# Kernel optimization log

Hardware: AMD Instinct MI355X
Metric: run time of the kernel (lower is better)

The kernel has to match this reference:

```python
import jax, jax.numpy as jnp
import numpy as np

DIM_MODEL = 512
KDIM = 64
NUM_FREQS = 70


def setup_inputs() -> dict:
    key = jax.random.key(0)
    ks = jax.random.split(key, 8)
    B, N = 8, 2048
    src = jax.random.normal(ks[0], (B, N, DIM_MODEL), dtype=jnp.float32)
    bias_tensor = jax.random.normal(ks[1], (N, N, 4), dtype=jnp.float32)
    multiplier = jax.random.uniform(ks[2], (B, N, N), dtype=jnp.float32)
    # f_theta_lc params
    W_r = jax.random.normal(ks[3], (NUM_FREQS, 2), dtype=jnp.float32)  # std=1.0 init
    C = jnp.ones((NUM_FREQS,), dtype=jnp.float32)
    log_p = jnp.float32(0.0)
    # Xavier-uniform attention projections (torch Linear weight layout [out, in])
    lim = float(np.sqrt(6.0 / (DIM_MODEL + KDIM)))
    W_q = jax.random.uniform(ks[4], (KDIM, DIM_MODEL), minval=-lim, maxval=lim, dtype=jnp.float32)
    W_k = jax.random.uniform(ks[5], (KDIM, DIM_MODEL), minval=-lim, maxval=lim, dtype=jnp.float32)
    W_v = jax.random.uniform(ks[6], (KDIM, DIM_MODEL), minval=-lim, maxval=lim, dtype=jnp.float32)
    s = jnp.float32(1.0)
    return {"src": src, "bias_tensor": bias_tensor, "multiplier": multiplier,
            "W_r": W_r, "C": C, "log_p": log_p,
            "W_q": W_q, "W_k": W_k, "W_v": W_v, "s": s}


def _f_theta(bias_tensor, W_r, C, log_p):
    # bias_tensor: [N, N, 4]; W_r: [F, 2]
    k1 = jnp.einsum('nmi,fi->nmf', bias_tensor[:, :, 0:2], W_r)
    k2 = jnp.einsum('nmi,fi->nmf', bias_tensor[:, :, 2:4], W_r)
    diff = jnp.cos(k1) + jnp.sin(k1) - jnp.cos(k2) - jnp.sin(k2)
    sigma = jnp.abs(jnp.sum(diff * C, axis=-1))  # [N, N]
    p = jnp.clip(jnp.exp(log_p), 0.5, 3.0)
    return jnp.exp(-jnp.power(sigma + 1e-6, p))


def reference(src, bias_tensor, multiplier, W_r, C, log_p, W_q, W_k, W_v, s):
    B = _f_theta(bias_tensor, W_r, C, log_p)  # [N, N]
    Q = jnp.einsum('bnd,kd->bnk', src, W_q)
    K = jnp.einsum('bnd,kd->bnk', src, W_k)
    V = jnp.einsum('bnd,kd->bnk', src, W_v)
    denom = jnp.sqrt(jnp.float32(KDIM))
    logits = (jnp.einsum('bnk,bmk->bnm', Q, K) + B[None]) / denom
    logits = logits * (s * multiplier)
    attn = jax.nn.softmax(logits, axis=-1)
    return jnp.einsum('bnm,bmk->bnk', attn, V)
```

## Files before the change

### kernel.cpp

```cpp
#include <hip/hip_runtime.h>
#include <hip/hip_bf16.h>

#define N_SEQ 2048
#define NB 8
#define DM 512
#define KD 64
#define NF 70

#define TG 512
#define TRANGE 6.5f
#define TSCL (511.0f / 13.0f)
#define TOFS (6.5f * TSCL)

typedef float f32x4 __attribute__((ext_vector_type(4)));
typedef short v8s  __attribute__((ext_vector_type(8)));

__device__ __forceinline__ ushort f2bf(float x) {
    uint u = __float_as_uint(x);
    return (ushort)((u + 0x7FFFu + ((u >> 16) & 1u)) >> 16);
}
__device__ __forceinline__ float bf2f(ushort h) {
    return __uint_as_float(((uint)h) << 16);
}
__device__ __forceinline__ uint cvtpk(float lo, float hi) {
    uint r;
    asm("v_cvt_pk_bf16_f32 %0, %1, %2" : "=v"(r) : "v"(lo), "v"(hi));
    return r;
}

__global__ __launch_bounds__(256) void tbuild_kernel(
    const float* __restrict__ Wr, const float* __restrict__ Cc,
    float4* __restrict__ T4)
{
    const float SQ2 = 1.41421356237309504880f;
    const float R2PI = 0.15915494309189533577f;
    int idx = blockIdx.x * 256 + threadIdx.x;
    int j = idx >> 9, i = idx & (TG - 1);
    const float h = 2.0f * TRANGE / (TG - 1);
    float y = -TRANGE + j * h;
    float x = -TRANGE + i * h;
    float g = 0.f;
    for (int f = 0; f < NF; ++f) {
        float w0 = Wr[2*f] * R2PI, w1 = Wr[2*f+1] * R2PI, cf = Cc[f];
        float k = __builtin_amdgcn_fractf(fmaf(x, w0, fmaf(y, w1, 0.125f)));
        g = fmaf(cf, __builtin_amdgcn_sinf(k), g);
    }
    g *= SQ2;
    float* T = (float*)T4;
    int ix = idx;
    T[4*ix + 0] = g;
    if (i > 0)               T[4*(ix - 1) + 1] = g;
    if (i == TG - 1)         T[4*ix + 1] = g;
    if (j > 0)               T[4*(ix - TG) + 2] = g;
    if (j == TG - 1)         T[4*ix + 2] = g;
    if (i > 0 && j > 0)      T[4*(ix - TG - 1) + 3] = g;
    if (i == TG - 1 && j > 0)         T[4*(ix - TG) + 3] = g;
    if (j == TG - 1 && i > 0)         T[4*(ix - 1) + 3] = g;
    if (i == TG - 1 && j == TG - 1)   T[4*ix + 3] = g;
}

#define QKV_BLOCKS 512

__global__ __launch_bounds__(256) void fat_kernel(
    const float* __restrict__ src, const float* __restrict__ Wq,
    const float* __restrict__ Wk, const float* __restrict__ Wv,
    ushort* __restrict__ Qh, ushort* __restrict__ Ql,
    ushort* __restrict__ Kh, ushort* __restrict__ VhT,
    const float* __restrict__ bias, const float4* __restrict__ T4,
    const float* __restrict__ logp, ushort* __restrict__ Bm)
{
    __shared__ ushort sS[32][72];
    __shared__ ushort sW[192][72];
    int tid = threadIdx.x;

    if (blockIdx.x < QKV_BLOCKS) {
        int lane = tid & 63, w = tid >> 6;
        int wr = w >> 1, wc = w & 1;
        int g = lane >> 4, ln = lane & 15;
        int row0 = blockIdx.x * 32;

        f32x4 acc[6];
#pragma unroll
        for (int t = 0; t < 6; ++t) acc[t] = {0.f, 0.f, 0.f, 0.f};

        for (int kc = 0; kc < 8; ++kc) {
            int k0 = kc * 64;
            __syncthreads();
            {
                int r = tid >> 3, c8 = (tid & 7) * 8;
                float4 f0 = *(const float4*)&src[(long)(row0 + r)*DM + k0 + c8];
                float4 f1 = *(const float4*)&src[(long)(row0 + r)*DM + k0 + c8 + 4];
                uint4 pk = make_uint4(cvtpk(f0.x, f0.y), cvtpk(f0.z, f0.w),
                                      cvtpk(f1.x, f1.y), cvtpk(f1.z, f1.w));
                *(uint4*)&sS[r][c8] = pk;
            }
            {
#pragma unroll
                for (int j = 0; j < 6; ++j) {
                    int slot = tid + j*256;
                    int r = slot >> 3, c8 = (slot & 7) * 8;
                    const float* Wp = (r < 64) ? Wq : (r < 128 ? Wk : Wv);
                    int rr = r & 63;
                    float4 f0 = *(const float4*)&Wp[(long)rr*DM + k0 + c8];
                    float4 f1 = *(const float4*)&Wp[(long)rr*DM + k0 + c8 + 4];
                    uint4 pk = make_uint4(cvtpk(f0.x, f0.y), cvtpk(f0.z, f0.w),
                                          cvtpk(f1.x, f1.y), cvtpk(f1.z, f1.w));
                    *(uint4*)&sW[r][c8] = pk;
                }
            }
            __syncthreads();
#pragma unroll
            for (int kw = 0; kw < 2; ++kw) {
                v8s bsrc = *(const v8s*)&sS[16*wr + ln][32*kw + 8*g];
#pragma unroll
                for (int t = 0; t < 6; ++t) {
                    v8s aw = *(const v8s*)&sW[96*wc + 16*t + ln][32*kw + 8*g];
                    acc[t] = __builtin_amdgcn_mfma_f32_16x16x32_bf16(aw, bsrc, acc[t], 0, 0, 0);
                }
            }
        }
        int n = row0 + 16*wr + ln;
        int bb = n >> 11, nn = n & 2047;
#pragma unroll
        for (int t = 0; t < 6; ++t) {
            int c0 = 96*wc + 16*t + 4*g;
            f32x4 v = acc[t];
            uint2 hp = make_uint2(cvtpk(v[0], v[1]), cvtpk(v[2], v[3]));
            if (c0 < 64) {
                *(uint2*)&Qh[(long)n*KD + c0] = hp;
                float h0 = __uint_as_float(hp.x << 16);
                float h1 = __uint_as_float(hp.x & 0xFFFF0000u);
                float h2 = __uint_as_float(hp.y << 16);
                float h3 = __uint_as_float(hp.y & 0xFFFF0000u);
                uint2 lp = make_uint2(cvtpk(v[0]-h0, v[1]-h1), cvtpk(v[2]-h2, v[3]-h3));
                *(uint2*)&Ql[(long)n*KD + c0] = lp;
            } else if (c0 < 128) {
                *(uint2*)&Kh[(long)n*KD + (c0 - 64)] = hp;
            } else {
                int kv = c0 - 128;
                VhT[((long)bb*KD + kv + 0)*N_SEQ + nn] = (ushort)(hp.x & 0xFFFFu);
                VhT[((long)bb*KD + kv + 1)*N_SEQ + nn] = (ushort)(hp.x >> 16);
                VhT[((long)bb*KD + kv + 2)*N_SEQ + nn] = (ushort)(hp.y & 0xFFFFu);
                VhT[((long)bb*KD + kv + 3)*N_SEQ + nn] = (ushort)(hp.y >> 16);
            }
        }
    } else {
        long base = (long)(blockIdx.x - QKV_BLOCKS) * 1024 + tid;
        float4 e[4];
        e[0] = ((const float4*)bias)[base];
        e[1] = ((const float4*)bias)[base + 256];
        e[2] = ((const float4*)bias)[base + 512];
        e[3] = ((const float4*)bias)[base + 768];

        float fu[8], fv[8]; float4 q[8];
#pragma unroll
        for (int k = 0; k < 8; ++k) {
            float x = (k & 1) ? e[k>>1].z : e[k>>1].x;
            float y = (k & 1) ? e[k>>1].w : e[k>>1].y;
            float u = fmaf(x, TSCL, TOFS);
            float v = fmaf(y, TSCL, TOFS);
            u = fminf(fmaxf(u, 0.0f), 510.999f);
            v = fminf(fmaxf(v, 0.0f), 510.999f);
            int iu = (int)u, iv = (int)v;
            fu[k] = __builtin_amdgcn_fractf(u);
            fv[k] = __builtin_amdgcn_fractf(v);
            q[k] = T4[iv * TG + iu];
        }
        float gq[8];
#pragma unroll
        for (int k = 0; k < 8; ++k) {
            float t0 = fmaf(fu[k], q[k].y - q[k].x, q[k].x);
            float t1 = fmaf(fu[k], q[k].w - q[k].z, q[k].z);
            gq[k] = fmaf(fv[k], t1 - t0, t0);
        }
        float p = __expf(logp[0]);
        p = fminf(fmaxf(p, 0.5f), 3.0f);
        if (p == 1.0f) {
#pragma unroll
            for (int k = 0; k < 4; ++k)
                Bm[base + 256*k] = f2bf(__expf(-(fabsf(gq[2*k] - gq[2*k+1]) + 1e-6f)));
        } else {
#pragma unroll
            for (int k = 0; k < 4; ++k)
                Bm[base + 256*k] = f2bf(__expf(-__powf(fabsf(gq[2*k] - gq[2*k+1]) + 1e-6f, p)));
        }
    }
}

__global__ __launch_bounds__(256, 4) void attn_mfma_kernel(
    const ushort* __restrict__ Qh, const ushort* __restrict__ Ql,
    const ushort* __restrict__ Kh, const ushort* __restrict__ VhT,
    const ushort* __restrict__ Bm, const float* __restrict__ mult,
    const float* __restrict__ sp,
    ushort* __restrict__ Opart, float* __restrict__ Mp, float* __restrict__ Lp)
{
    __shared__ ushort sKh[64][72];
    __shared__ ushort sVT[64][72];
    __shared__ ushort sP[4][16][72];

    int tid = threadIdx.x;
    int lane = tid & 63, w = tid >> 6;
    int g = lane >> 4, ln = lane & 15;
    int bid = blockIdx.x;
    int b = bid & 7, rest = bid >> 3, p = rest & 3, nt = rest >> 2;
    int n0 = nt * 64;

    int qrow = n0 + w*16 + ln;
    long qoff = ((long)b*N_SEQ + qrow)*KD + 8*g;
    v8s qh0 = *(const v8s*)&Qh[qoff];
    v8s qh1 = *(const v8s*)&Qh[qoff + 32];
    v8s ql0 = *(const v8s*)&Ql[qoff];
    v8s ql1 = *(const v8s*)&Ql[qoff + 32];

    float s  = sp[0];
    float qs = 0.125f * s * 1.44269504088896340736f;
    float M = -1e30f, L = 0.f;
    f32x4 accO[4];
#pragma unroll
    for (int i = 0; i < 4; ++i) accO[i] = {0.f, 0.f, 0.f, 0.f};

    long brow = (long)qrow * N_SEQ;
    long urow = ((long)b*N_SEQ + qrow) * N_SEQ;
    long vtb  = (long)b*KD*N_SEQ;
    long kbB  = (long)b*N_SEQ*KD;

    int srow = tid >> 3, sc8 = (tid & 7) * 8;

    uint4 rKh0, rKh1, rVT0, rVT1;
    ushort4 nBq[4]; float4 nUq[4];
    {
        int m0 = p*512;
        rKh0 = *(const uint4*)&Kh[kbB + (long)(m0+srow)*KD + sc8];
        rKh1 = *(const uint4*)&Kh[kbB + (long)(m0+srow+32)*KD + sc8];
        rVT0 = *(const uint4*)&VhT[vtb + (long)srow*N_SEQ + m0 + sc8];
        rVT1 = *(const uint4*)&VhT[vtb + (long)(srow+32)*N_SEQ + m0 + sc8];
#pragma unroll
        for (int sub = 0; sub < 4; ++sub) {
            nBq[sub] = *(const ushort4*)&Bm[brow + m0 + 16*sub + 4*g];
            nUq[sub] = *(const float4*)&mult[urow + m0 + 16*sub + 4*g];
        }
    }

    for (int mt = 0; mt < 8; ++mt) {
        int m0 = p*512 + mt*64;
        __syncthreads();
        *(uint4*)&sKh[srow][sc8]      = rKh0;
        *(uint4*)&sKh[srow + 32][sc8] = rKh1;
        *(uint4*)&sVT[srow][sc8]      = rVT0;
        *(uint4*)&sVT[srow + 32][sc8] = rVT1;
        __syncthreads();

        if (mt < 7) {
            int m1 = m0 + 64;
            rKh0 = *(const uint4*)&Kh[kbB + (long)(m1+srow)*KD + sc8];
            rKh1 = *(const uint4*)&Kh[kbB + (long)(m1+srow+32)*KD + sc8];
            rVT0 = *(const uint4*)&VhT[vtb + (long)srow*N_SEQ + m1 + sc8];
            rVT1 = *(const uint4*)&VhT[vtb + (long)(srow+32)*N_SEQ + m1 + sc8];
        }

        f32x4 S[4];
#pragma unroll
        for (int i = 0; i < 4; ++i) S[i] = {0.f, 0.f, 0.f, 0.f};
        __builtin_amdgcn_s_setprio(1);
#pragma unroll
        for (int ks = 0; ks < 2; ++ks) {
            v8s qh = ks ? qh1 : qh0;
            v8s ql = ks ? ql1 : ql0;
#pragma unroll
            for (int sub = 0; sub < 4; ++sub) {
                v8s kh = *(const v8s*)&sKh[16*sub + ln][32*ks + 8*g];
                S[sub] = __builtin_amdgcn_mfma_f32_16x16x32_bf16(kh, qh, S[sub], 0, 0, 0);
                S[sub] = __builtin_amdgcn_mfma_f32_16x16x32_bf16(kh, ql, S[sub], 0, 0, 0);
            }
        }
        __builtin_amdgcn_s_setprio(0);

        float lg[16]; float mx = -1e30f;
#pragma unroll
        for (int sub = 0; sub < 4; ++sub) {
            float b0 = bf2f(nBq[sub].x), b1 = bf2f(nBq[sub].y);
            float b2 = bf2f(nBq[sub].z), b3 = bf2f(nBq[sub].w);
            lg[4*sub+0] = (S[sub][0] + b0) * nUq[sub].x * qs;
            lg[4*sub+1] = (S[sub][1] + b1) * nUq[sub].y * qs;
            lg[4*sub+2] = (S[sub][2] + b2) * nUq[sub].z * qs;
            lg[4*sub+3] = (S[sub][3] + b3) * nUq[sub].w * qs;
            mx = fmaxf(mx, fmaxf(fmaxf(lg[4*sub+0], lg[4*sub+1]),
                                 fmaxf(lg[4*sub+2], lg[4*sub+3])));
        }
        if (mt < 7) {
            int m1 = m0 + 64;
#pragma unroll
            for (int sub = 0; sub < 4; ++sub) {
                nBq[sub] = *(const ushort4*)&Bm[brow + m1 + 16*sub + 4*g];
                nUq[sub] = *(const float4*)&mult[urow + m1 + 16*sub + 4*g];
            }
        }
        mx = fmaxf(mx, __shfl_xor(mx, 16));
        mx = fmaxf(mx, __shfl_xor(mx, 32));
        float Mn = fmaxf(M, mx);
        float sc = __builtin_amdgcn_exp2f(M - Mn);
        float ps = 0.f;
#pragma unroll
        for (int i = 0; i < 16; ++i) {
            float e = __builtin_amdgcn_exp2f(lg[i] - Mn);
            lg[i] = e; ps += e;
        }
        ps += __shfl_xor(ps, 16);
        ps += __shfl_xor(ps, 32);
        L = L * sc + ps; M = Mn;

#pragma unroll
        for (int sub = 0; sub < 4; ++sub) {
            uint2 pk = make_uint2(cvtpk(lg[4*sub+0], lg[4*sub+1]),
                                  cvtpk(lg[4*sub+2], lg[4*sub+3]));
            *(uint2*)&sP[w][ln][16*sub + 4*g] = pk;
        }

#pragma unroll
        for (int i = 0; i < 4; ++i) accO[i] *= sc;
        __builtin_amdgcn_s_setprio(1);
#pragma unroll
        for (int ks = 0; ks < 2; ++ks) {
            v8s pp = *(const v8s*)&sP[w][ln][32*ks + 8*g];
#pragma unroll
            for (int sub = 0; sub < 4; ++sub) {
                v8s vh = *(const v8s*)&sVT[16*sub + ln][32*ks + 8*g];
                accO[sub] = __builtin_amdgcn_mfma_f32_16x16x32_bf16(vh, pp, accO[sub], 0, 0, 0);
            }
        }
        __builtin_amdgcn_s_setprio(0);
    }

    long ob = ((long)bid*64 + (w*16 + ln)) * 64;
#pragma unroll
    for (int sub = 0; sub < 4; ++sub) {
        uint2 pk = make_uint2(cvtpk(accO[sub][0], accO[sub][1]),
                              cvtpk(accO[sub][2], accO[sub][3]));
        *(uint2*)&Opart[ob + 16*sub + 4*g] = pk;
    }
    if (g == 0) {
        Mp[bid*64 + w*16 + ln] = M;
        Lp[bid*64 + w*16 + ln] = L;
    }
}

__global__ __launch_bounds__(256) void combine_kernel(
    const ushort* __restrict__ Opart, const float* __restrict__ Mp,
    const float* __restrict__ Lp, float* __restrict__ out)
{
    int idx = blockIdx.x * 256 + threadIdx.x;
    int kq = idx & 15;
    int row = idx >> 4;
    int b = row >> 11, n = row & 2047;
    int nt = n >> 6, r = n & 63;
    int bid0 = ((nt*4) << 3) | b;
    float Mq[4], Lq[4];
#pragma unroll
    for (int p = 0; p < 4; ++p) {
        Mq[p] = Mp[(bid0 + 8*p)*64 + r];
        Lq[p] = Lp[(bid0 + 8*p)*64 + r];
    }
    float Mx = fmaxf(fmaxf(Mq[0], Mq[1]), fmaxf(Mq[2], Mq[3]));
    float4 acc = make_float4(0.f, 0.f, 0.f, 0.f);
    float Ls = 0.f;
#pragma unroll
    for (int p = 0; p < 4; ++p) {
        float e = __builtin_amdgcn_exp2f(Mq[p] - Mx);
        Ls += Lq[p] * e;
        ushort4 o = *(const ushort4*)&Opart[((long)(bid0 + 8*p)*64 + r)*64 + 4*kq];
        acc.x = fmaf(e, bf2f(o.x), acc.x);
        acc.y = fmaf(e, bf2f(o.y), acc.y);
        acc.z = fmaf(e, bf2f(o.z), acc.z);
        acc.w = fmaf(e, bf2f(o.w), acc.w);
    }
    float inv = 1.0f / Ls;
    float4 o;
    o.x = acc.x * inv; o.y = acc.y * inv;
    o.z = acc.z * inv; o.w = acc.w * inv;
    *(float4*)&out[(long)row*64 + 4*kq] = o;
}

extern "C" void kernel_launch(void* const* d_in, const int* in_sizes, int n_in,
                              void* d_out, int out_size, void* d_ws, size_t ws_size,
                              hipStream_t stream) {
    const float* src  = (const float*)d_in[0];
    const float* bias = (const float*)d_in[1];
    const float* mult = (const float*)d_in[2];
    const float* Wr   = (const float*)d_in[3];
    const float* Cc   = (const float*)d_in[4];
    const float* logp = (const float*)d_in[5];
    const float* Wq   = (const float*)d_in[6];
    const float* Wk   = (const float*)d_in[7];
    const float* Wv   = (const float*)d_in[8];
    const float* sp   = (const float*)d_in[9];
    float* outp = (float*)d_out;

    const size_t QKV_E = (size_t)NB * N_SEQ * KD;
    ushort* wsu = (ushort*)d_ws;
    ushort* Bm  = wsu;
    ushort* Qh  = wsu + (size_t)N_SEQ * N_SEQ;
    ushort* Ql  = Qh + QKV_E;
    ushort* Kh  = Ql + QKV_E;
    ushort* VhT = Kh + QKV_E;
    ushort* Opart = VhT + QKV_E;
    float* Mp = (float*)(Opart + (size_t)1024 * 64 * 64);
    float* Lp = Mp + (size_t)1024 * 64;
    float4* T4 = (float4*)(Lp + (size_t)1024 * 64);

    tbuild_kernel<<<(TG*TG)/256, 256, 0, stream>>>(Wr, Cc, T4);
    fat_kernel<<<QKV_BLOCKS + 4096, 256, 0, stream>>>(
        src, Wq, Wk, Wv, Qh, Ql, Kh, VhT, bias, T4, logp, Bm);
    attn_mfma_kernel<<<1024, 256, 0, stream>>>(Qh, Ql, Kh, VhT, Bm, mult, sp,
                                               Opart, Mp, Lp);
    combine_kernel<<<1024, 256, 0, stream>>>(Opart, Mp, Lp, outp);
}
```

Baseline: 107.3 us.

## Widen QKV projection tiles and prefetch bias/multiplier two tiles ahead

The QKV projection blocks now handle 64 rows each instead of 32. Each wave computes all 192 output columns, which halves the number of blocks and the redundant weight loads per row. The attention loop double-buffers the bias and multiplier register prefetch so loads are issued two tiles ahead, and the loop is fully unrolled to keep the buffer index static. This hides more of the latency of the large multiplier stream, at the cost of more registers and possibly lower occupancy.

```diff
diff --git a/kernel.cpp b/kernel.cpp
--- a/kernel.cpp
+++ b/kernel.cpp
@@ -59,7 +59,7 @@
     if (i == TG - 1 && j == TG - 1)   T[4*ix + 3] = g;
 }
 
-#define QKV_BLOCKS 512
+#define QKV_BLOCKS 256
 
 __global__ __launch_bounds__(256) void fat_kernel(
     const float* __restrict__ src, const float* __restrict__ Wq,
@@ -69,35 +69,38 @@
     const float* __restrict__ bias, const float4* __restrict__ T4,
     const float* __restrict__ logp, ushort* __restrict__ Bm)
 {
-    __shared__ ushort sS[32][72];
+    __shared__ ushort sS[64][72];
     __shared__ ushort sW[192][72];
     int tid = threadIdx.x;
 
     if (blockIdx.x < QKV_BLOCKS) {
         int lane = tid & 63, w = tid >> 6;
-        int wr = w >> 1, wc = w & 1;
         int g = lane >> 4, ln = lane & 15;
-        int row0 = blockIdx.x * 32;
-
-        f32x4 acc[6];
-#pragma unroll
-        for (int t = 0; t < 6; ++t) acc[t] = {0.f, 0.f, 0.f, 0.f};
+        int row0 = blockIdx.x * 64;
+
+        f32x4 acc[12];
+#pragma unroll
+        for (int t = 0; t < 12; ++t) acc[t] = {0.f, 0.f, 0.f, 0.f};
 
         for (int kc = 0; kc < 8; ++kc) {
             int k0 = kc * 64;
             __syncthreads();
             {
-                int r = tid >> 3, c8 = (tid & 7) * 8;
-                float4 f0 = *(const float4*)&src[(long)(row0 + r)*DM + k0 + c8];
-                float4 f1 = *(const float4*)&src[(long)(row0 + r)*DM + k0 + c8 + 4];
-                uint4 pk = make_uint4(cvtpk(f0.x, f0.y), cvtpk(f0.z, f0.w),
-                                      cvtpk(f1.x, f1.y), cvtpk(f1.z, f1.w));
-                *(uint4*)&sS[r][c8] = pk;
+#pragma unroll
+                for (int jj = 0; jj < 2; ++jj) {
+                    int slot = tid + jj*256;
+                    int r = slot >> 3, c8 = (slot & 7) * 8;
+                    float4 f0 = *(const float4*)&src[(long)(row0 + r)*DM + k0 + c8];
+                    float4 f1 = *(const float4*)&src[(long)(row0 + r)*DM + k0 + c8 + 4];
+                    uint4 pk = make_uint4(cvtpk(f0.x, f0.y), cvtpk(f0.z, f0.w),
+                                          cvtpk(f1.x, f1.y), cvtpk(f1.z, f1.w));
+                    *(uint4*)&sS[r][c8] = pk;
+                }
             }
             {
 #pragma unroll
-                for (int j = 0; j < 6; ++j) {
-                    int slot = tid + j*256;
+                for (int jj = 0; jj < 6; ++jj) {
+                    int slot = tid + jj*256;
                     int r = slot >> 3, c8 = (slot & 7) * 8;
                     const float* Wp = (r < 64) ? Wq : (r < 128 ? Wk : Wv);
                     int rr = r & 63;
@@ -111,19 +114,19 @@
             __syncthreads();
 #pragma unroll
             for (int kw = 0; kw < 2; ++kw) {
-                v8s bsrc = *(const v8s*)&sS[16*wr + ln][32*kw + 8*g];
-#pragma unroll
-                for (int t = 0; t < 6; ++t) {
-                    v8s aw = *(const v8s*)&sW[96*wc + 16*t + ln][32*kw + 8*g];
+                v8s bsrc = *(const v8s*)&sS[16*w + ln][32*kw + 8*g];
+#pragma unroll
+                for (int t = 0; t < 12; ++t) {
+                    v8s aw = *(const v8s*)&sW[16*t + ln][32*kw + 8*g];
                     acc[t] = __builtin_amdgcn_mfma_f32_16x16x32_bf16(aw, bsrc, acc[t], 0, 0, 0);
                 }
             }
         }
-        int n = row0 + 16*wr + ln;
+        int n = row0 + 16*w + ln;
         int bb = n >> 11, nn = n & 2047;
 #pragma unroll
-        for (int t = 0; t < 6; ++t) {
-            int c0 = 96*wc + 16*t + 4*g;
+        for (int t = 0; t < 12; ++t) {
+            int c0 = 16*t + 4*g;
             f32x4 v = acc[t];
             uint2 hp = make_uint2(cvtpk(v[0], v[1]), cvtpk(v[2], v[3]));
             if (c0 < 64) {
@@ -227,7 +230,7 @@
     int srow = tid >> 3, sc8 = (tid & 7) * 8;
 
     uint4 rKh0, rKh1, rVT0, rVT1;
-    ushort4 nBq[4]; float4 nUq[4];
+    ushort4 nBq[2][4]; float4 nUq[2][4];
     {
         int m0 = p*512;
         rKh0 = *(const uint4*)&Kh[kbB + (long)(m0+srow)*KD + sc8];
@@ -235,13 +238,19 @@
         rVT0 = *(const uint4*)&VhT[vtb + (long)srow*N_SEQ + m0 + sc8];
         rVT1 = *(const uint4*)&VhT[vtb + (long)(srow+32)*N_SEQ + m0 + sc8];
 #pragma unroll
-        for (int sub = 0; sub < 4; ++sub) {
-            nBq[sub] = *(const ushort4*)&Bm[brow + m0 + 16*sub + 4*g];
-            nUq[sub] = *(const float4*)&mult[urow + m0 + 16*sub + 4*g];
-        }
-    }
-
+        for (int d = 0; d < 2; ++d) {
+            int md = m0 + d*64;
+#pragma unroll
+            for (int sub = 0; sub < 4; ++sub) {
+                nBq[d][sub] = *(const ushort4*)&Bm[brow + md + 16*sub + 4*g];
+                nUq[d][sub] = *(const float4*)&mult[urow + md + 16*sub + 4*g];
+            }
+        }
+    }
+
+#pragma unroll
     for (int mt = 0; mt < 8; ++mt) {
+        const int cur = mt & 1;
         int m0 = p*512 + mt*64;
         __syncthreads();
         *(uint4*)&sKh[srow][sc8]      = rKh0;
@@ -278,21 +287,21 @@
         float lg[16]; float mx = -1e30f;
 #pragma unroll
         for (int sub = 0; sub < 4; ++sub) {
-            float b0 = bf2f(nBq[sub].x), b1 = bf2f(nBq[sub].y);
-            float b2 = bf2f(nBq[sub].z), b3 = bf2f(nBq[sub].w);
-            lg[4*sub+0] = (S[sub][0] + b0) * nUq[sub].x * qs;
-            lg[4*sub+1] = (S[sub][1] + b1) * nUq[sub].y * qs;
-            lg[4*sub+2] = (S[sub][2] + b2) * nUq[sub].z * qs;
-            lg[4*sub+3] = (S[sub][3] + b3) * nUq[sub].w * qs;
+            float b0 = bf2f(nBq[cur][sub].x), b1 = bf2f(nBq[cur][sub].y);
+            float b2 = bf2f(nBq[cur][sub].z), b3 = bf2f(nBq[cur][sub].w);
+            lg[4*sub+0] = (S[sub][0] + b0) * nUq[cur][sub].x * qs;
+            lg[4*sub+1] = (S[sub][1] + b1) * nUq[cur][sub].y * qs;
+            lg[4*sub+2] = (S[sub][2] + b2) * nUq[cur][sub].z * qs;
+            lg[4*sub+3] = (S[sub][3] + b3) * nUq[cur][sub].w * qs;
             mx = fmaxf(mx, fmaxf(fmaxf(lg[4*sub+0], lg[4*sub+1]),
                                  fmaxf(lg[4*sub+2], lg[4*sub+3])));
         }
-        if (mt < 7) {
-            int m1 = m0 + 64;
+        if (mt < 6) {
+            int m2 = m0 + 128;
 #pragma unroll
             for (int sub = 0; sub < 4; ++sub) {
-                nBq[sub] = *(const ushort4*)&Bm[brow + m1 + 16*sub + 4*g];
-                nUq[sub] = *(const float4*)&mult[urow + m1 + 16*sub + 4*g];
+                nBq[cur][sub] = *(const ushort4*)&Bm[brow + m2 + 16*sub + 4*g];
+                nUq[cur][sub] = *(const float4*)&mult[urow + m2 + 16*sub + 4*g];
             }
         }
         mx = fmaxf(mx, __shfl_xor(mx, 16));
```

After: 155.0 us. +44.5%, slower.
